# Optimization experiments

Measured on AMD Instinct MI355X. Metric: run time of the kernel, lower is better.

## Reference

```python
import jax, jax.numpy as jnp
import numpy as np

IN_FEATURES = 48
OUT_FEATURES = 64
ALPHA = 0.2  # LeakyReLU negative slope
NUM_INTENT = 16
N = 8192


def setup_inputs() -> dict:
    key = jax.random.key(0)
    k1, k2, k3, k4, k5 = jax.random.split(key, 5)
    # Xavier-uniform-ish params (exact init doesn't matter for correctness testing)
    W = jax.random.uniform(k1, (IN_FEATURES, OUT_FEATURES), jnp.float32, -0.3, 0.3)
    a = jax.random.uniform(k2, (2 * OUT_FEATURES, 1), jnp.float32, -0.3, 0.3)
    intent_interaction = jax.random.normal(k3, (NUM_INTENT, NUM_INTENT), jnp.float32) * 0.1
    intent_alpha = jnp.asarray(0.1, jnp.float32)
    inp = jax.random.normal(k4, (N, IN_FEATURES), jnp.float32)
    adj = jnp.ones((N, N), jnp.float32)  # unused by the math, kept for signature fidelity
    intent_labels = jax.random.randint(k5, (N,), 0, NUM_INTENT, jnp.int64 if jax.config.jax_enable_x64 else jnp.int32)
    return {"input": inp, "adj": adj, "W": W, "a": a,
            "intent_interaction": intent_interaction, "intent_alpha": intent_alpha,
            "intent_labels": intent_labels}


def reference(input, adj, W, a, intent_interaction, intent_alpha, intent_labels):
    h = input @ W                       # [N, F]
    F_ = h.shape[1]
    a1 = a[:F_, 0]                      # source part of attention vector
    a2 = a[F_:, 0]                      # target part
    # e[i,j] = leakyrelu(a1.h_i + a2.h_j) without materializing [N,N,2F]
    s1 = h @ a1                         # [N]
    s2 = h @ a2                         # [N]
    spatial_e = jax.nn.leaky_relu(s1[:, None] + s2[None, :], negative_slope=ALPHA)
    # intent bias: gather from interaction matrix, no python loops
    idx = jnp.clip(intent_labels - 1, 0, NUM_INTENT - 1)
    intent_bias = intent_interaction[idx[:, None], idx[None, :]]  # [N, N]
    total_e = spatial_e + intent_alpha * intent_bias
    # NOTE: original softmaxes over dim=0 (columns) and does NOT mask with adj
    attention = jax.nn.softmax(total_e, axis=0)
    h_prime = attention @ h             # [N, F]
    return jax.nn.elu(h_prime)          # concat=True path
```

## Files before the change

### kernel.cpp

```cpp
#include <hip/hip_runtime.h>
#include <hip/hip_bf16.h>

#define NN 8192
#define FF 64
#define INF 48
#define NP 8704
#define NCH (NP/32)
#define LOG2E 1.4426950408889634f

typedef __attribute__((ext_vector_type(8))) short short8;
typedef __attribute__((ext_vector_type(4))) float f32x4;

__device__ __forceinline__ float fexp2(float x) { return __builtin_amdgcn_exp2f(x); }

__device__ __forceinline__ unsigned int packbf2(float a, float b) {
  union { __hip_bfloat162 h2; unsigned int u; } c;
  c.h2 = __float22bfloat162_rn(float2{a, b});
  return c.u;
}
__device__ __forceinline__ unsigned short packbf1(float a) {
  union { __hip_bfloat16 h; unsigned short u; } c;
  c.h = __float2bfloat16(a);
  return c.u;
}
__device__ __forceinline__ float elu(float v) { return v > 0.f ? v : __expf(v) - 1.f; }

__global__ __launch_bounds__(256) void kA(const float* __restrict__ in,
                                          const float* __restrict__ W,
                                          const float* __restrict__ a,
                                          const int* __restrict__ labels,
                                          float* __restrict__ h,
                                          float* __restrict__ s1,
                                          float* __restrict__ s2,
                                          int* __restrict__ ci) {
  __shared__ float sIn[4][INF];
  int t = threadIdx.x;
  int w = t >> 6, lane = t & 63;
  int i = blockIdx.x * 4 + w;
  if (lane < INF) sIn[w][lane] = in[i * INF + lane];
  __syncthreads();
  float acc = 0.f;
#pragma unroll
  for (int k = 0; k < INF; k++) acc += sIn[w][k] * W[k * FF + lane];
  h[i * FF + lane] = acc;
  float v1 = acc * a[lane];
  float v2 = acc * a[FF + lane];
#pragma unroll
  for (int off = 32; off > 0; off >>= 1) {
    v1 += __shfl_xor(v1, off, 64);
    v2 += __shfl_xor(v2, off, 64);
  }
  if (lane == 0) {
    s1[i] = v1 * LOG2E;
    s2[i] = v2 * LOG2E;
    int c = labels[i] - 1;
    ci[i] = c < 0 ? 0 : (c > 15 ? 15 : c);
  }
}

__global__ __launch_bounds__(1024) void kSort(const float* __restrict__ s1,
                                              const float* __restrict__ s2,
                                              const int* __restrict__ ci,
                                              int* __restrict__ perm,
                                              float* __restrict__ s1p,
                                              float* __restrict__ s2p,
                                              int* __restrict__ clsc) {
  __shared__ int wcnt[16][16];
  __shared__ int wbase[16][16];
  __shared__ int tot[16];
  __shared__ int cbase[17];
  int t = threadIdx.x;
  int wv = t >> 6, lane = t & 63;
  unsigned long long lower = (1ULL << lane) - 1;
  int c[8], myoff[8];
  float v1[8], v2[8];
#pragma unroll
  for (int k = 0; k < 8; k++) {
    int i = wv * 512 + k * 64 + lane;
    c[k] = ci[i];
    v1[k] = s1[i];
    v2[k] = s2[i];
  }
#pragma unroll 1
  for (int cls = 0; cls < 16; cls++) {
    int run = 0;
#pragma unroll
    for (int k = 0; k < 8; k++) {
      unsigned long long m = __ballot(c[k] == cls);
      if (c[k] == cls) myoff[k] = run + __popcll(m & lower);
      run += __popcll(m);
    }
    if (lane == 0) wcnt[wv][cls] = run;
  }
  __syncthreads();
  if (t < 16) {
    int s = 0;
    for (int w = 0; w < 16; w++) { wbase[w][t] = s; s += wcnt[w][t]; }
    tot[t] = s;
  }
  __syncthreads();
  if (t == 0) {
    int s = 0;
    for (int cls = 0; cls < 16; cls++) { cbase[cls] = s; s += (tot[cls] + 31) & ~31; }
    cbase[16] = s;
  }
  __syncthreads();
#pragma unroll
  for (int k = 0; k < 8; k++) {
    int i = wv * 512 + k * 64 + lane;
    int pos = cbase[c[k]] + wbase[wv][c[k]] + myoff[k];
    perm[pos] = i;
    s1p[pos] = v1[k];
    s2p[pos] = v2[k];
    clsc[pos >> 5] = c[k];
  }
  int S = cbase[16];
#pragma unroll 1
  for (int cls = 0; cls < 16; cls++) {
    int start = cbase[cls] + tot[cls];
    int end = (cls < 15) ? cbase[cls + 1] : S;
    if (t < end - start) {
      int pos = start + t;
      perm[pos] = -1;
      s1p[pos] = -100.f;
      s2p[pos] = -100.f;
      clsc[pos >> 5] = cls;
    }
  }
  if (S + t < NP) {
    int pos = S + t;
    perm[pos] = -1;
    s1p[pos] = -100.f;
    s2p[pos] = -100.f;
  }
  if (t < NCH - (S >> 5)) clsc[(S >> 5) + t] = 0;
}

__global__ __launch_bounds__(256) void kDE(const float* __restrict__ s1p,
                                           const float* __restrict__ s2p,
                                           const int* __restrict__ clsc,
                                           const float* __restrict__ h,
                                           const int* __restrict__ perm,
                                           const float* __restrict__ Bmat,
                                           const float* __restrict__ alpha_p,
                                           unsigned short* __restrict__ h2T) {
  __shared__ float EBT[256];
  __shared__ int clsL[NCH];
  __shared__ float red[8][33];
  __shared__ float Dinv[32];
  __shared__ int permL[32];
  int t = threadIdx.x;
  int blk = blockIdx.x;
  int jp0 = blk * 32;
  EBT[t] = __expf(alpha_p[0] * Bmat[t]);
  clsL[t] = clsc[t];
  if (t < NCH - 256) clsL[256 + t] = clsc[256 + t];
  if (t < 32) permL[t] = perm[jp0 + t];
  __syncthreads();
  int c = t & 31, rseg = t >> 5;
  float s2j = s2p[jp0 + c];
  int cj = clsL[blk];
  float acc = 0.f;
#pragma unroll 1
  for (int ch = 0; ch < 34; ch++) {
    int chunk = rseg * 34 + ch;
    float w = EBT[clsL[chunk] * 16 + cj];
    int base = chunk * 32;
    float p = 0.f;
#pragma unroll
    for (int q = 0; q < 8; q++) {
      float4 sv = *(const float4*)&s1p[base + q * 4];
      float x0 = sv.x + s2j, x1 = sv.y + s2j, x2 = sv.z + s2j, x3 = sv.w + s2j;
      p += fexp2(fmaxf(x0, 0.2f * x0));
      p += fexp2(fmaxf(x1, 0.2f * x1));
      p += fexp2(fmaxf(x2, 0.2f * x2));
      p += fexp2(fmaxf(x3, 0.2f * x3));
    }
    acc = fmaf(p, w, acc);
  }
  red[rseg][c] = acc;
  __syncthreads();
  if (t < 32) {
    float s = 0.f;
#pragma unroll
    for (int r = 0; r < 8; r++) s += red[r][t];
    Dinv[t] = 1.0f / s;
  }
  __syncthreads();
  int p = permL[c];
  int fb = rseg * 8;
  if (p < 0) {
#pragma unroll
    for (int k = 0; k < 8; k++) h2T[(size_t)(fb + k) * NP + jp0 + c] = 0;
  } else {
    float g = Dinv[c];
    float4 h0 = *(const float4*)&h[p * FF + fb];
    float4 h1 = *(const float4*)&h[p * FF + fb + 4];
    h2T[(size_t)(fb + 0) * NP + jp0 + c] = packbf1(g * h0.x);
    h2T[(size_t)(fb + 1) * NP + jp0 + c] = packbf1(g * h0.y);
    h2T[(size_t)(fb + 2) * NP + jp0 + c] = packbf1(g * h0.z);
    h2T[(size_t)(fb + 3) * NP + jp0 + c] = packbf1(g * h0.w);
    h2T[(size_t)(fb + 4) * NP + jp0 + c] = packbf1(g * h1.x);
    h2T[(size_t)(fb + 5) * NP + jp0 + c] = packbf1(g * h1.y);
    h2T[(size_t)(fb + 6) * NP + jp0 + c] = packbf1(g * h1.z);
    h2T[(size_t)(fb + 7) * NP + jp0 + c] = packbf1(g * h1.w);
  }
}

__global__ __launch_bounds__(256) void kF2(const float* __restrict__ s1,
                                           const int* __restrict__ ci,
                                           const float* __restrict__ s2p,
                                           const int* __restrict__ clsc,
                                           const unsigned short* __restrict__ h2T,
                                           const float* __restrict__ Bmat,
                                           const float* __restrict__ alpha_p,
                                           float* __restrict__ out) {
  __shared__ float EBT2[256];
  __shared__ float red[3 * 1088];
  int t = threadIdx.x;
  int wv = t >> 6, lane = t & 63;
  int quad = lane >> 4, l16 = lane & 15;
  EBT2[t] = __expf(alpha_p[0] * Bmat[(t & 15) * 16 + (t >> 4)]);
  int row0 = blockIdx.x * 16;
  float s1v = s1[row0 + l16];
  int civ = ci[row0 + l16];
  __syncthreads();

  f32x4 acc0 = {0.f, 0.f, 0.f, 0.f};
  f32x4 acc1 = {0.f, 0.f, 0.f, 0.f};
  f32x4 acc2 = {0.f, 0.f, 0.f, 0.f};
  f32x4 acc3 = {0.f, 0.f, 0.f, 0.f};

  int jbeg = wv * (NP / 4);
  int jend = jbeg + (NP / 4);
  for (int j0 = jbeg; j0 < jend; j0 += 32) {
    int cch = clsc[j0 >> 5];
    float w = EBT2[cch * 16 + civ];
    float4 sa = *(const float4*)&s2p[j0 + quad * 8];
    float4 sb = *(const float4*)&s2p[j0 + quad * 8 + 4];
    float e0, e1, e2, e3, e4, e5, e6, e7, x;
    x = s1v + sa.x; e0 = fexp2(fmaxf(x, 0.2f * x)) * w;
    x = s1v + sa.y; e1 = fexp2(fmaxf(x, 0.2f * x)) * w;
    x = s1v + sa.z; e2 = fexp2(fmaxf(x, 0.2f * x)) * w;
    x = s1v + sa.w; e3 = fexp2(fmaxf(x, 0.2f * x)) * w;
    x = s1v + sb.x; e4 = fexp2(fmaxf(x, 0.2f * x)) * w;
    x = s1v + sb.y; e5 = fexp2(fmaxf(x, 0.2f * x)) * w;
    x = s1v + sb.z; e6 = fexp2(fmaxf(x, 0.2f * x)) * w;
    x = s1v + sb.w; e7 = fexp2(fmaxf(x, 0.2f * x)) * w;
    union { short8 s; unsigned int u[4]; } af;
    af.u[0] = packbf2(e0, e1);
    af.u[1] = packbf2(e2, e3);
    af.u[2] = packbf2(e4, e5);
    af.u[3] = packbf2(e6, e7);
    const unsigned short* bbase = h2T + (size_t)l16 * NP + j0 + quad * 8;
    short8 b0 = *(const short8*)(bbase);
    short8 b1 = *(const short8*)(bbase + 16 * NP);
    short8 b2 = *(const short8*)(bbase + 32 * NP);
    short8 b3 = *(const short8*)(bbase + 48 * NP);
    acc0 = __builtin_amdgcn_mfma_f32_16x16x32_bf16(af.s, b0, acc0, 0, 0, 0);
    acc1 = __builtin_amdgcn_mfma_f32_16x16x32_bf16(af.s, b1, acc1, 0, 0, 0);
    acc2 = __builtin_amdgcn_mfma_f32_16x16x32_bf16(af.s, b2, acc2, 0, 0, 0);
    acc3 = __builtin_amdgcn_mfma_f32_16x16x32_bf16(af.s, b3, acc3, 0, 0, 0);
  }
  if (wv > 0) {
    int base = (wv - 1) * 1088 + lane * 17;
#pragma unroll
    for (int reg = 0; reg < 4; reg++) {
      red[base + reg] = acc0[reg];
      red[base + 4 + reg] = acc1[reg];
      red[base + 8 + reg] = acc2[reg];
      red[base + 12 + reg] = acc3[reg];
    }
  }
  __syncthreads();
  if (wv == 0) {
    int base = lane * 17;
#pragma unroll
    for (int reg = 0; reg < 4; reg++) {
      float v0 = acc0[reg] + red[base + reg] + red[1088 + base + reg] + red[2176 + base + reg];
      float v1 = acc1[reg] + red[base + 4 + reg] + red[1088 + base + 4 + reg] + red[2176 + base + 4 + reg];
      float v2 = acc2[reg] + red[base + 8 + reg] + red[1088 + base + 8 + reg] + red[2176 + base + 8 + reg];
      float v3 = acc3[reg] + red[base + 12 + reg] + red[1088 + base + 12 + reg] + red[2176 + base + 12 + reg];
      int ro = (row0 + quad * 4 + reg) * FF + l16;
      out[ro + 0] = elu(v0);
      out[ro + 16] = elu(v1);
      out[ro + 32] = elu(v2);
      out[ro + 48] = elu(v3);
    }
  }
}

extern "C" void kernel_launch(void* const* d_in, const int* in_sizes, int n_in,
                              void* d_out, int out_size, void* d_ws, size_t ws_size,
                              hipStream_t stream) {
  const float* in = (const float*)d_in[0];
  const float* W = (const float*)d_in[2];
  const float* a = (const float*)d_in[3];
  const float* Bmat = (const float*)d_in[4];
  const float* alpha = (const float*)d_in[5];
  const int* labels = (const int*)d_in[6];
  float* out = (float*)d_out;

  float* ws = (float*)d_ws;
  float* h = ws;
  float* s1 = h + 524288;
  float* s2 = s1 + 8192;
  int* ci = (int*)(s2 + 8192);
  float* s1p = (float*)(ci + 8192);
  float* s2p = s1p + NP;
  int* perm = (int*)(s2p + NP);
  int* clsc = perm + NP;
  int* pad = clsc + NCH;
  unsigned short* h2T = (unsigned short*)(pad + 16);

  kA<<<2048, 256, 0, stream>>>(in, W, a, labels, h, s1, s2, ci);
  kSort<<<1, 1024, 0, stream>>>(s1, s2, ci, perm, s1p, s2p, clsc);
  kDE<<<NCH, 256, 0, stream>>>(s1p, s2p, clsc, h, perm, Bmat, alpha, h2T);
  kF2<<<512, 256, 0, stream>>>(s1, ci, s2p, clsc, h2T, Bmat, alpha, out);
}
```

Before: 430.0 us.

## Replace dense N×N attention with per-class sorted prefix sums and binary search

```diff
diff --git a/kernel.cpp b/kernel.cpp
--- a/kernel.cpp
+++ b/kernel.cpp
@@ -1,37 +1,22 @@
 #include <hip/hip_runtime.h>
-#include <hip/hip_bf16.h>
 
 #define NN 8192
 #define FF 64
 #define INF 48
-#define NP 8704
-#define NCH (NP/32)
+#define NC 16
+#define CAP 2048
 #define LOG2E 1.4426950408889634f
 
-typedef __attribute__((ext_vector_type(8))) short short8;
-typedef __attribute__((ext_vector_type(4))) float f32x4;
-
 __device__ __forceinline__ float fexp2(float x) { return __builtin_amdgcn_exp2f(x); }
-
-__device__ __forceinline__ unsigned int packbf2(float a, float b) {
-  union { __hip_bfloat162 h2; unsigned int u; } c;
-  c.h2 = __float22bfloat162_rn(float2{a, b});
-  return c.u;
-}
-__device__ __forceinline__ unsigned short packbf1(float a) {
-  union { __hip_bfloat16 h; unsigned short u; } c;
-  c.h = __float2bfloat16(a);
-  return c.u;
-}
 __device__ __forceinline__ float elu(float v) { return v > 0.f ? v : __expf(v) - 1.f; }
 
-__global__ __launch_bounds__(256) void kA(const float* __restrict__ in,
+__global__ __launch_bounds__(256) void k1(const float* __restrict__ in,
                                           const float* __restrict__ W,
                                           const float* __restrict__ a,
                                           const int* __restrict__ labels,
                                           float* __restrict__ h,
-                                          float* __restrict__ s1,
-                                          float* __restrict__ s2,
+                                          float* __restrict__ s1L,
+                                          float* __restrict__ s2L,
                                           int* __restrict__ ci) {
   __shared__ float sIn[4][INF];
   int t = threadIdx.x;
@@ -51,243 +36,296 @@
     v2 += __shfl_xor(v2, off, 64);
   }
   if (lane == 0) {
-    s1[i] = v1 * LOG2E;
-    s2[i] = v2 * LOG2E;
+    s1L[i] = v1 * LOG2E;
+    s2L[i] = v2 * LOG2E;
     int c = labels[i] - 1;
     ci[i] = c < 0 ? 0 : (c > 15 ? 15 : c);
   }
 }
 
-__global__ __launch_bounds__(1024) void kSort(const float* __restrict__ s1,
-                                              const float* __restrict__ s2,
-                                              const int* __restrict__ ci,
-                                              int* __restrict__ perm,
-                                              float* __restrict__ s1p,
-                                              float* __restrict__ s2p,
-                                              int* __restrict__ clsc) {
+__global__ __launch_bounds__(1024) void k2(const float* __restrict__ s1L,
+                                           const float* __restrict__ s2L,
+                                           const int* __restrict__ ci,
+                                           int* __restrict__ offG,
+                                           float* __restrict__ s1s,
+                                           float* __restrict__ sufA,
+                                           float* __restrict__ preB,
+                                           float* __restrict__ s2s,
+                                           int* __restrict__ perm2,
+                                           float* __restrict__ ea2,
+                                           float* __restrict__ eb2) {
   __shared__ int wcnt[16][16];
-  __shared__ int wbase[16][16];
   __shared__ int tot[16];
-  __shared__ int cbase[17];
+  __shared__ int offL[17];
+  __shared__ int idxL[CAP];
+  __shared__ float key[CAP];
+  __shared__ int pay[CAP];
+  __shared__ float exA[CAP];
+  __shared__ float exB[CAP];
+  __shared__ float wred[32];
+  __shared__ float wexA[17], wexB[17];
+  __shared__ int gcnt;
   int t = threadIdx.x;
   int wv = t >> 6, lane = t & 63;
-  unsigned long long lower = (1ULL << lane) - 1;
-  int c[8], myoff[8];
-  float v1[8], v2[8];
-#pragma unroll
-  for (int k = 0; k < 8; k++) {
-    int i = wv * 512 + k * 64 + lane;
-    c[k] = ci[i];
-    v1[k] = s1[i];
-    v2[k] = s2[i];
-  }
+  int myc = blockIdx.x;
+  unsigned long long lower = (1ULL << lane) - 1ULL;
+  int c8[8];
+#pragma unroll
+  for (int k = 0; k < 8; k++) c8[k] = ci[wv * 512 + k * 64 + lane];
+  if (t == 0) gcnt = 0;
 #pragma unroll 1
   for (int cls = 0; cls < 16; cls++) {
     int run = 0;
 #pragma unroll
-    for (int k = 0; k < 8; k++) {
-      unsigned long long m = __ballot(c[k] == cls);
-      if (c[k] == cls) myoff[k] = run + __popcll(m & lower);
-      run += __popcll(m);
-    }
+    for (int k = 0; k < 8; k++) run += __popcll(__ballot(c8[k] == cls));
     if (lane == 0) wcnt[wv][cls] = run;
   }
   __syncthreads();
   if (t < 16) {
     int s = 0;
-    for (int w = 0; w < 16; w++) { wbase[w][t] = s; s += wcnt[w][t]; }
+#pragma unroll
+    for (int w = 0; w < 16; w++) s += wcnt[w][t];
     tot[t] = s;
   }
   __syncthreads();
   if (t == 0) {
     int s = 0;
-    for (int cls = 0; cls < 16; cls++) { cbase[cls] = s; s += (tot[cls] + 31) & ~31; }
-    cbase[16] = s;
-  }
-  __syncthreads();
+    for (int c = 0; c < 16; c++) { offL[c] = s; s += tot[c]; }
+    offL[16] = s;
+  }
+  __syncthreads();
+  if (myc == 0 && t < 17) offG[t] = offL[t];
+  int moff = offL[myc], msz = tot[myc];
+  int offE = moff + myc;
 #pragma unroll
   for (int k = 0; k < 8; k++) {
-    int i = wv * 512 + k * 64 + lane;
-    int pos = cbase[c[k]] + wbase[wv][c[k]] + myoff[k];
-    perm[pos] = i;
-    s1p[pos] = v1[k];
-    s2p[pos] = v2[k];
-    clsc[pos >> 5] = c[k];
-  }
-  int S = cbase[16];
-#pragma unroll 1
-  for (int cls = 0; cls < 16; cls++) {
-    int start = cbase[cls] + tot[cls];
-    int end = (cls < 15) ? cbase[cls + 1] : S;
-    if (t < end - start) {
-      int pos = start + t;
-      perm[pos] = -1;
-      s1p[pos] = -100.f;
-      s2p[pos] = -100.f;
-      clsc[pos >> 5] = cls;
-    }
-  }
-  if (S + t < NP) {
-    int pos = S + t;
-    perm[pos] = -1;
-    s1p[pos] = -100.f;
-    s2p[pos] = -100.f;
-  }
-  if (t < NCH - (S >> 5)) clsc[(S >> 5) + t] = 0;
-}
-
-__global__ __launch_bounds__(256) void kDE(const float* __restrict__ s1p,
-                                           const float* __restrict__ s2p,
-                                           const int* __restrict__ clsc,
-                                           const float* __restrict__ h,
-                                           const int* __restrict__ perm,
-                                           const float* __restrict__ Bmat,
-                                           const float* __restrict__ alpha_p,
-                                           unsigned short* __restrict__ h2T) {
+    bool is = (c8[k] == myc);
+    unsigned long long m = __ballot(is);
+    int cnt = __popcll(m);
+    int base = 0;
+    if (lane == 0 && cnt) base = atomicAdd(&gcnt, cnt);
+    base = __shfl(base, 0, 64);
+    if (is) idxL[base + __popcll(m & lower)] = wv * 512 + k * 64 + lane;
+  }
+  __syncthreads();
+  int C = (msz <= 1024) ? 1024 : CAP;
+  for (int m = t; m < C; m += 1024) key[m] = (m < msz) ? s1L[idxL[m]] : 3.0e38f;
+  __syncthreads();
+  for (int kk = 2; kk <= C; kk <<= 1) {
+    for (int jj = kk >> 1; jj > 0; jj >>= 1) {
+      for (int i = t; i < C; i += 1024) {
+        int l = i ^ jj;
+        if (l > i) {
+          float av = key[i], bv = key[l];
+          if ((av > bv) == ((i & kk) == 0)) { key[i] = bv; key[l] = av; }
+        }
+      }
+      __syncthreads();
+    }
+  }
+  for (int m = t; m < CAP; m += 1024) {
+    bool in = m < msz;
+    float kv = in ? key[m] : 0.f;
+    if (in) s1s[moff + m] = kv;
+    exA[m] = in ? fexp2(kv) : 0.f;
+    exB[m] = in ? fexp2(0.2f * kv) : 0.f;
+  }
+  __syncthreads();
+  float v0 = exA[2 * t], v1 = exA[2 * t + 1];
+  float u0 = exB[2 * t], u1 = exB[2 * t + 1];
+  float ts = v0 + v1, us = u0 + u1;
+  float tsi = ts, usi = us;
+#pragma unroll
+  for (int d = 1; d < 64; d <<= 1) {
+    float nA = __shfl_up(tsi, d, 64);
+    float nB = __shfl_up(usi, d, 64);
+    if (lane >= d) { tsi += nA; usi += nB; }
+  }
+  if (lane == 63) { wred[wv] = tsi; wred[16 + wv] = usi; }
+  __syncthreads();
+  if (t == 0) {
+    float sA = 0.f, sB = 0.f;
+    for (int w = 0; w < 16; w++) { wexA[w] = sA; wexB[w] = sB; sA += wred[w]; sB += wred[16 + w]; }
+    wexA[16] = sA; wexB[16] = sB;
+  }
+  __syncthreads();
+  float eAr = wexA[wv] + (tsi - ts);
+  float eBr = wexB[wv] + (usi - us);
+  exA[2 * t] = eAr; exA[2 * t + 1] = eAr + v0;
+  exB[2 * t] = eBr; exB[2 * t + 1] = eBr + u0;
+  __syncthreads();
+  float totA = wexA[16];
+  for (int k = t; k <= msz; k += 1024) {
+    sufA[offE + k] = totA - exA[k];
+    preB[offE + k] = exB[k];
+  }
+  for (int m = t; m < C; m += 1024) {
+    bool in = m < msz;
+    key[m] = in ? s2L[idxL[m]] : 3.0e38f;
+    pay[m] = in ? idxL[m] : -1;
+  }
+  __syncthreads();
+  for (int kk = 2; kk <= C; kk <<= 1) {
+    for (int jj = kk >> 1; jj > 0; jj >>= 1) {
+      for (int i = t; i < C; i += 1024) {
+        int l = i ^ jj;
+        if (l > i) {
+          float av = key[i], bv = key[l];
+          if ((av > bv) == ((i & kk) == 0)) {
+            key[i] = bv; key[l] = av;
+            int pt = pay[i]; pay[i] = pay[l]; pay[l] = pt;
+          }
+        }
+      }
+      __syncthreads();
+    }
+  }
+  for (int m = t; m < msz; m += 1024) {
+    float kv = key[m];
+    s2s[moff + m] = kv;
+    perm2[moff + m] = pay[m];
+    ea2[moff + m] = fexp2(kv);
+    eb2[moff + m] = fexp2(0.2f * kv);
+  }
+}
+
+__global__ __launch_bounds__(256) void k3(const float* __restrict__ s1L,
+                                          const float* __restrict__ s2L,
+                                          const int* __restrict__ ci,
+                                          const int* __restrict__ offG,
+                                          const float* __restrict__ s1s,
+                                          const float* __restrict__ sufA,
+                                          const float* __restrict__ preB,
+                                          const float* __restrict__ s2s,
+                                          const float* __restrict__ Bmat,
+                                          const float* __restrict__ alphap,
+                                          float* __restrict__ Dinv,
+                                          int* __restrict__ kt) {
   __shared__ float EBT[256];
-  __shared__ int clsL[NCH];
-  __shared__ float red[8][33];
-  __shared__ float Dinv[32];
-  __shared__ int permL[32];
-  int t = threadIdx.x;
+  __shared__ int offL[17];
+  int t = threadIdx.x;
+  EBT[t] = __expf(alphap[0] * Bmat[t]);
+  if (t < 17) offL[t] = offG[t];
+  __syncthreads();
+  int c = t & 15, il = t >> 4;
+  int o = offL[c], n = offL[c + 1] - o;
   int blk = blockIdx.x;
-  int jp0 = blk * 32;
-  EBT[t] = __expf(alpha_p[0] * Bmat[t]);
-  clsL[t] = clsc[t];
-  if (t < NCH - 256) clsL[256 + t] = clsc[256 + t];
-  if (t < 32) permL[t] = perm[jp0 + t];
-  __syncthreads();
-  int c = t & 31, rseg = t >> 5;
-  float s2j = s2p[jp0 + c];
-  int cj = clsL[blk];
+  if (blk < 512) {
+    int j = blk * 16 + il;
+    float s2v = s2L[j];
+    int cj = ci[j];
+    float keyv = -s2v;
+    int lo = 0, len = n;
+    while (len > 0) {
+      int half = len >> 1;
+      int mid = lo + half;
+      if (s1s[o + mid] <= keyv) { lo = mid + 1; len -= half + 1; }
+      else len = half;
+    }
+    int b = o + c + lo;
+    float term = EBT[c * 16 + cj] * fmaf(fexp2(s2v), sufA[b], fexp2(0.2f * s2v) * preB[b]);
+#pragma unroll
+    for (int d = 1; d < 16; d <<= 1) term += __shfl_xor(term, d, 64);
+    if (c == 0) Dinv[j] = 1.0f / term;
+  } else {
+    int i = (blk - 512) * 16 + il;
+    float keyv = -s1L[i];
+    int lo = 0, len = n;
+    while (len > 0) {
+      int half = len >> 1;
+      int mid = lo + half;
+      if (s2s[o + mid] <= keyv) { lo = mid + 1; len -= half + 1; }
+      else len = half;
+    }
+    kt[i * NC + c] = lo;
+  }
+}
+
+__global__ __launch_bounds__(512) void k4(const int* __restrict__ offG,
+                                          const int* __restrict__ perm2,
+                                          const float* __restrict__ ea2,
+                                          const float* __restrict__ eb2,
+                                          const float* __restrict__ Dinv,
+                                          const float* __restrict__ h,
+                                          float* __restrict__ sufG1,
+                                          float* __restrict__ preG2) {
+  __shared__ float ps[8][64];
+  __shared__ int offL[17];
+  int t = threadIdx.x;
+  int wv = t >> 6, f = t & 63;
+  if (t < 17) offL[t] = offG[t];
+  __syncthreads();
+  int cls = blockIdx.x;
+  int o = offL[cls], sz = offL[cls + 1] - o, oE = o + cls;
+  int type = wv >> 2, w4 = wv & 3;
+  int L = (sz + 3) >> 2;
+  int m0 = w4 * L;
+  int m1 = m0 + L;
+  if (m1 > sz) m1 = sz;
+  if (m0 > sz) m0 = sz;
   float acc = 0.f;
-#pragma unroll 1
-  for (int ch = 0; ch < 34; ch++) {
-    int chunk = rseg * 34 + ch;
-    float w = EBT[clsL[chunk] * 16 + cj];
-    int base = chunk * 32;
-    float p = 0.f;
-#pragma unroll
-    for (int q = 0; q < 8; q++) {
-      float4 sv = *(const float4*)&s1p[base + q * 4];
-      float x0 = sv.x + s2j, x1 = sv.y + s2j, x2 = sv.z + s2j, x3 = sv.w + s2j;
-      p += fexp2(fmaxf(x0, 0.2f * x0));
-      p += fexp2(fmaxf(x1, 0.2f * x1));
-      p += fexp2(fmaxf(x2, 0.2f * x2));
-      p += fexp2(fmaxf(x3, 0.2f * x3));
-    }
-    acc = fmaf(p, w, acc);
-  }
-  red[rseg][c] = acc;
-  __syncthreads();
-  if (t < 32) {
-    float s = 0.f;
-#pragma unroll
-    for (int r = 0; r < 8; r++) s += red[r][t];
-    Dinv[t] = 1.0f / s;
-  }
-  __syncthreads();
-  int p = permL[c];
-  int fb = rseg * 8;
-  if (p < 0) {
-#pragma unroll
-    for (int k = 0; k < 8; k++) h2T[(size_t)(fb + k) * NP + jp0 + c] = 0;
+  if (type == 0) {
+    for (int m = m1 - 1; m >= m0; m--) {
+      int j = perm2[o + m];
+      acc += ea2[o + m] * Dinv[j] * h[j * FF + f];
+    }
   } else {
-    float g = Dinv[c];
-    float4 h0 = *(const float4*)&h[p * FF + fb];
-    float4 h1 = *(const float4*)&h[p * FF + fb + 4];
-    h2T[(size_t)(fb + 0) * NP + jp0 + c] = packbf1(g * h0.x);
-    h2T[(size_t)(fb + 1) * NP + jp0 + c] = packbf1(g * h0.y);
-    h2T[(size_t)(fb + 2) * NP + jp0 + c] = packbf1(g * h0.z);
-    h2T[(size_t)(fb + 3) * NP + jp0 + c] = packbf1(g * h0.w);
-    h2T[(size_t)(fb + 4) * NP + jp0 + c] = packbf1(g * h1.x);
-    h2T[(size_t)(fb + 5) * NP + jp0 + c] = packbf1(g * h1.y);
-    h2T[(size_t)(fb + 6) * NP + jp0 + c] = packbf1(g * h1.z);
-    h2T[(size_t)(fb + 7) * NP + jp0 + c] = packbf1(g * h1.w);
-  }
-}
-
-__global__ __launch_bounds__(256) void kF2(const float* __restrict__ s1,
-                                           const int* __restrict__ ci,
-                                           const float* __restrict__ s2p,
-                                           const int* __restrict__ clsc,
-                                           const unsigned short* __restrict__ h2T,
-                                           const float* __restrict__ Bmat,
-                                           const float* __restrict__ alpha_p,
-                                           float* __restrict__ out) {
-  __shared__ float EBT2[256];
-  __shared__ float red[3 * 1088];
-  int t = threadIdx.x;
-  int wv = t >> 6, lane = t & 63;
-  int quad = lane >> 4, l16 = lane & 15;
-  EBT2[t] = __expf(alpha_p[0] * Bmat[(t & 15) * 16 + (t >> 4)]);
-  int row0 = blockIdx.x * 16;
-  float s1v = s1[row0 + l16];
-  int civ = ci[row0 + l16];
-  __syncthreads();
-
-  f32x4 acc0 = {0.f, 0.f, 0.f, 0.f};
-  f32x4 acc1 = {0.f, 0.f, 0.f, 0.f};
-  f32x4 acc2 = {0.f, 0.f, 0.f, 0.f};
-  f32x4 acc3 = {0.f, 0.f, 0.f, 0.f};
-
-  int jbeg = wv * (NP / 4);
-  int jend = jbeg + (NP / 4);
-  for (int j0 = jbeg; j0 < jend; j0 += 32) {
-    int cch = clsc[j0 >> 5];
-    float w = EBT2[cch * 16 + civ];
-    float4 sa = *(const float4*)&s2p[j0 + quad * 8];
-    float4 sb = *(const float4*)&s2p[j0 + quad * 8 + 4];
-    float e0, e1, e2, e3, e4, e5, e6, e7, x;
-    x = s1v + sa.x; e0 = fexp2(fmaxf(x, 0.2f * x)) * w;
-    x = s1v + sa.y; e1 = fexp2(fmaxf(x, 0.2f * x)) * w;
-    x = s1v + sa.z; e2 = fexp2(fmaxf(x, 0.2f * x)) * w;
-    x = s1v + sa.w; e3 = fexp2(fmaxf(x, 0.2f * x)) * w;
-    x = s1v + sb.x; e4 = fexp2(fmaxf(x, 0.2f * x)) * w;
-    x = s1v + sb.y; e5 = fexp2(fmaxf(x, 0.2f * x)) * w;
-    x = s1v + sb.z; e6 = fexp2(fmaxf(x, 0.2f * x)) * w;
-    x = s1v + sb.w; e7 = fexp2(fmaxf(x, 0.2f * x)) * w;
-    union { short8 s; unsigned int u[4]; } af;
-    af.u[0] = packbf2(e0, e1);
-    af.u[1] = packbf2(e2, e3);
-    af.u[2] = packbf2(e4, e5);
-    af.u[3] = packbf2(e6, e7);
-    const unsigned short* bbase = h2T + (size_t)l16 * NP + j0 + quad * 8;
-    short8 b0 = *(const short8*)(bbase);
-    short8 b1 = *(const short8*)(bbase + 16 * NP);
-    short8 b2 = *(const short8*)(bbase + 32 * NP);
-    short8 b3 = *(const short8*)(bbase + 48 * NP);
-    acc0 = __builtin_amdgcn_mfma_f32_16x16x32_bf16(af.s, b0, acc0, 0, 0, 0);
-    acc1 = __builtin_amdgcn_mfma_f32_16x16x32_bf16(af.s, b1, acc1, 0, 0, 0);
-    acc2 = __builtin_amdgcn_mfma_f32_16x16x32_bf16(af.s, b2, acc2, 0, 0, 0);
-    acc3 = __builtin_amdgcn_mfma_f32_16x16x32_bf16(af.s, b3, acc3, 0, 0, 0);
-  }
-  if (wv > 0) {
-    int base = (wv - 1) * 1088 + lane * 17;
-#pragma unroll
-    for (int reg = 0; reg < 4; reg++) {
-      red[base + reg] = acc0[reg];
-      red[base + 4 + reg] = acc1[reg];
-      red[base + 8 + reg] = acc2[reg];
-      red[base + 12 + reg] = acc3[reg];
-    }
-  }
-  __syncthreads();
-  if (wv == 0) {
-    int base = lane * 17;
-#pragma unroll
-    for (int reg = 0; reg < 4; reg++) {
-      float v0 = acc0[reg] + red[base + reg] + red[1088 + base + reg] + red[2176 + base + reg];
-      float v1 = acc1[reg] + red[base + 4 + reg] + red[1088 + base + 4 + reg] + red[2176 + base + 4 + reg];
-      float v2 = acc2[reg] + red[base + 8 + reg] + red[1088 + base + 8 + reg] + red[2176 + base + 8 + reg];
-      float v3 = acc3[reg] + red[base + 12 + reg] + red[1088 + base + 12 + reg] + red[2176 + base + 12 + reg];
-      int ro = (row0 + quad * 4 + reg) * FF + l16;
-      out[ro + 0] = elu(v0);
-      out[ro + 16] = elu(v1);
-      out[ro + 32] = elu(v2);
-      out[ro + 48] = elu(v3);
-    }
-  }
+    for (int m = m0; m < m1; m++) {
+      int j = perm2[o + m];
+      acc += eb2[o + m] * Dinv[j] * h[j * FF + f];
+    }
+  }
+  ps[wv][f] = acc;
+  __syncthreads();
+  if (type == 0) {
+    float run = 0.f;
+    for (int w = w4 + 1; w < 4; w++) run += ps[w][f];
+    for (int m = m1 - 1; m >= m0; m--) {
+      int j = perm2[o + m];
+      run += ea2[o + m] * Dinv[j] * h[j * FF + f];
+      sufG1[(oE + m) * FF + f] = run;
+    }
+    if (wv == 0) sufG1[(oE + sz) * FF + f] = 0.f;
+  } else {
+    float run = 0.f;
+    for (int w = 0; w < w4; w++) run += ps[4 + w][f];
+    for (int m = m0; m < m1; m++) {
+      int j = perm2[o + m];
+      preG2[(oE + m) * FF + f] = run;
+      run += eb2[o + m] * Dinv[j] * h[j * FF + f];
+    }
+    if (w4 == 3) preG2[(oE + sz) * FF + f] = run;
+  }
+}
+
+__global__ __launch_bounds__(256) void k5(const float* __restrict__ s1L,
+                                          const int* __restrict__ ci,
+                                          const int* __restrict__ offG,
+                                          const int* __restrict__ kt,
+                                          const float* __restrict__ sufG1,
+                                          const float* __restrict__ preG2,
+                                          const float* __restrict__ Bmat,
+                                          const float* __restrict__ alphap,
+                                          float* __restrict__ out) {
+  __shared__ float EBT[256];
+  __shared__ int offL[17];
+  int t = threadIdx.x;
+  EBT[t] = __expf(alphap[0] * Bmat[t]);
+  if (t < 17) offL[t] = offG[t];
+  __syncthreads();
+  int wv = t >> 6, f = t & 63;
+  int i = blockIdx.x * 4 + wv;
+  float s1v = s1L[i];
+  int ai = ci[i];
+  float e1 = fexp2(s1v), e1b = fexp2(0.2f * s1v);
+  float acc = 0.f;
+#pragma unroll
+  for (int c = 0; c < NC; c++) {
+    int k = kt[i * NC + c];
+    int base = (offL[c] + c + k) * FF + f;
+    acc = fmaf(EBT[ai * 16 + c], fmaf(e1, sufG1[base], e1b * preG2[base]), acc);
+  }
+  out[i * FF + f] = elu(acc);
 }
 
 extern "C" void kernel_launch(void* const* d_in, const int* in_sizes, int n_in,
@@ -303,18 +341,25 @@
 
   float* ws = (float*)d_ws;
   float* h = ws;
-  float* s1 = h + 524288;
-  float* s2 = s1 + 8192;
-  int* ci = (int*)(s2 + 8192);
-  float* s1p = (float*)(ci + 8192);
-  float* s2p = s1p + NP;
-  int* perm = (int*)(s2p + NP);
-  int* clsc = perm + NP;
-  int* pad = clsc + NCH;
-  unsigned short* h2T = (unsigned short*)(pad + 16);
-
-  kA<<<2048, 256, 0, stream>>>(in, W, a, labels, h, s1, s2, ci);
-  kSort<<<1, 1024, 0, stream>>>(s1, s2, ci, perm, s1p, s2p, clsc);
-  kDE<<<NCH, 256, 0, stream>>>(s1p, s2p, clsc, h, perm, Bmat, alpha, h2T);
-  kF2<<<512, 256, 0, stream>>>(s1, ci, s2p, clsc, h2T, Bmat, alpha, out);
-}
+  float* s1L = h + 524288;
+  float* s2L = s1L + 8192;
+  int* ci = (int*)(s2L + 8192);
+  int* offG = ci + 8192;
+  float* s1s = (float*)(offG + 32);
+  float* sufA = s1s + 8192;
+  float* preB = sufA + 8224;
+  float* s2s = preB + 8224;
+  int* perm2 = (int*)(s2s + 8192);
+  float* ea2 = (float*)(perm2 + 8192);
+  float* eb2 = ea2 + 8192;
+  float* Dinv = eb2 + 8192;
+  int* kt = (int*)(Dinv + 8192);
+  float* sufG1 = (float*)(kt + 131072);
+  float* preG2 = sufG1 + 8224 * 64;
+
+  k1<<<2048, 256, 0, stream>>>(in, W, a, labels, h, s1L, s2L, ci);
+  k2<<<16, 1024, 0, stream>>>(s1L, s2L, ci, offG, s1s, sufA, preB, s2s, perm2, ea2, eb2);
+  k3<<<1024, 256, 0, stream>>>(s1L, s2L, ci, offG, s1s, sufA, preB, s2s, Bmat, alpha, Dinv, kt);
+  k4<<<16, 512, 0, stream>>>(offG, perm2, ea2, eb2, Dinv, h, sufG1, preG2);
+  k5<<<2048, 256, 0, stream>>>(s1L, ci, offG, kt, sufG1, preG2, Bmat, alpha, out);
+}
```

New measurement: 537.1 us. +24.9%, slower.
